# Performance work log

Measured on AMD Instinct MI355X. Metric: run time of the kernel, lower is better.

The kernel has to match this reference:

```python
import jax, jax.numpy as jnp
import numpy as np

H = 516      # LSTM hidden per direction
T = 512      # encoder source length
B = 64       # batch
NY = 20      # decoder target length
SEQ = 20     # seqLen == decoder input feature == n classes


def _u(key, shape, k):
    return jax.random.uniform(key, shape, jnp.float32, -k, k)


def setup_inputs() -> dict:
    key = jax.random.key(0)
    ks = jax.random.split(key, 26)
    kh = float(1.0 / np.sqrt(H))
    ka = float(1.0 / np.sqrt(2 * H * 2))
    inp = {}
    inp['x'] = jax.random.normal(ks[0], (T, B, 4), jnp.float32)
    inp['y'] = jax.random.normal(ks[1], (NY, B, SEQ), jnp.float32)
    inp['label'] = jax.random.randint(ks[2], (NY, B), 0, SEQ)
    inp['expand_W'] = _u(ks[3], (256, 4), 0.5)
    inp['expand_b'] = _u(ks[4], (256,), 0.5)
    # encoder biLSTM: 2 layers x 2 directions; PyTorch gate order i,f,g,o
    inp['eWi0'] = _u(ks[5], (2, 4 * H, 256), kh)
    inp['eWh0'] = _u(ks[6], (2, 4 * H, H), kh)
    inp['eb0'] = _u(ks[7], (2, 4 * H), kh)
    inp['eWi1'] = _u(ks[8], (2, 4 * H, 2 * H), kh)
    inp['eWh1'] = _u(ks[9], (2, 4 * H, H), kh)
    inp['eb1'] = _u(ks[10], (2, 4 * H), kh)
    # decoder biLSTM
    inp['dWi0'] = _u(ks[11], (2, 4 * H, SEQ), kh)
    inp['dWh0'] = _u(ks[12], (2, 4 * H, H), kh)
    inp['db0'] = _u(ks[13], (2, 4 * H), kh)
    inp['dWi1'] = _u(ks[14], (2, 4 * H, 2 * H), kh)
    inp['dWh1'] = _u(ks[15], (2, 4 * H, H), kh)
    inp['db1'] = _u(ks[16], (2, 4 * H), kh)
    # concat attention: Linear(2064, 1032) + v
    inp['attn_W'] = _u(ks[17], (2 * H, 4 * H), ka)
    inp['attn_b'] = _u(ks[18], (2 * H,), ka)
    inp['attn_v'] = _u(ks[19], (2 * H,), ka)
    inp['concat_W'] = _u(ks[20], (2 * H, 4 * H), ka)
    inp['concat_b'] = _u(ks[21], (2 * H,), ka)
    inp['out_W'] = _u(ks[22], (SEQ, 2 * H), float(1.0 / np.sqrt(2 * H)))
    inp['out_b'] = _u(ks[23], (SEQ,), float(1.0 / np.sqrt(2 * H)))
    return inp


def _cell(x, h, c, Wi, Wh, b):
    g = x @ Wi.T + h @ Wh.T + b
    i, f, gg, o = jnp.split(g, 4, axis=-1)
    c2 = jax.nn.sigmoid(f) * c + jax.nn.sigmoid(i) * jnp.tanh(gg)
    h2 = jax.nn.sigmoid(o) * jnp.tanh(c2)
    return h2, c2


def _run_dir(xs, h0, c0, Wi, Wh, b, reverse):
    def step(carry, xt):
        h, c = _cell(xt, carry[0], carry[1], Wi, Wh, b)
        return (h, c), h
    (hT, cT), ys = jax.lax.scan(step, (h0, c0), xs, reverse=reverse)
    return ys, hT, cT


def _bilstm(xs, Wi0, Wh0, b0, Wi1, Wh1, b1):
    z = jnp.zeros((xs.shape[1], H), xs.dtype)
    out = xs
    hs, cs = [], []
    for Wi, Wh, b in ((Wi0, Wh0, b0), (Wi1, Wh1, b1)):
        yf, hf, cf = _run_dir(out, z, z, Wi[0], Wh[0], b[0], False)
        yb, hb, cb = _run_dir(out, z, z, Wi[1], Wh[1], b[1], True)
        out = jnp.concatenate([yf, yb], -1)
        hs += [hf, hb]
        cs += [cf, cb]
    return out, jnp.stack(hs), jnp.stack(cs)


def reference(x, y, label, expand_W, expand_b, eWi0, eWh0, eb0, eWi1, eWh1, eb1,
              dWi0, dWh0, db0, dWi1, dWh1, db1, attn_W, attn_b, attn_v,
              concat_W, concat_b, out_W, out_b):
    xe = x @ expand_W.T + expand_b                       # [T,B,256]
    outenc, h0, c0 = _bilstm(xe, eWi0, eWh0, eb0, eWi1, eWh1, eb1)  # [T,B,1032],[4,B,H]
    lab = label.astype(jnp.int32)

    def dec_step(carry, inp):
        h, c, loss = carry
        yi, li = inp                                    # [B,SEQ], [B]
        # 1-step bidirectional 2-layer decoder LSTM (seq len 1 => fwd==bwd path)
        h0f, c0f = _cell(yi, h[0], c[0], dWi0[0], dWh0[0], db0[0])
        h0b, c0b = _cell(yi, h[1], c[1], dWi0[1], dWh0[1], db0[1])
        l0 = jnp.concatenate([h0f, h0b], -1)
        h1f, c1f = _cell(l0, h[2], c[2], dWi1[0], dWh1[0], db1[0])
        h1b, c1b = _cell(l0, h[3], c[3], dWi1[1], dWh1[1], db1[1])
        outdec = jnp.concatenate([h1f, h1b], -1)        # [B,1032]
        # concat attention over encoder outputs
        hid = jnp.broadcast_to(outdec[None], outenc.shape)
        energy = jnp.tanh(jnp.concatenate([hid, outenc], -1) @ attn_W.T + attn_b)
        score = jnp.einsum('h,tbh->tb', attn_v, energy)
        aw = jax.nn.softmax(score, axis=0)              # softmax over src_len
        context = jnp.einsum('tb,tbh->bh', aw, outenc)
        co = jnp.tanh(jnp.concatenate([outdec, context], -1) @ concat_W.T + concat_b)
        logits = co @ out_W.T + out_b                   # [B,SEQ]
        ls = jax.nn.log_softmax(logits, -1)
        ce = -jnp.take_along_axis(ls, li[:, None], 1).mean()
        h_new = jnp.stack([h0f, h0b, h1f, h1b])
        c_new = jnp.stack([c0f, c0b, c1f, c1b])
        return (h_new, c_new, loss + ce), None

    init = (h0, c0, jnp.float32(0.0))
    (_, _, loss), _ = jax.lax.scan(dec_step, init, (y, lab))
    return loss
```

## Files before the change

### kernel.cpp

```cpp
#include <hip/hip_runtime.h>
#include <hip/hip_bf16.h>
#include <cstdint>

typedef __attribute__((ext_vector_type(8))) short s8v;
typedef __attribute__((ext_vector_type(4))) float f4v;

#define DEV __device__ __forceinline__

constexpr int Hh  = 516;
constexpr int HP  = 544;
constexpr int FH  = 2064;
constexpr int NP  = 2176;
constexpr int TT  = 512;
constexpr int BB  = 64;
constexpr int LD2 = 1088;
constexpr int LDE = 1152;
constexpr int CS  = 528;
constexpr int XR  = 584;

DEV float bf2f(unsigned short u){ return __builtin_bit_cast(float, (unsigned)u<<16); }
DEV unsigned short f2bf(float f){
  unsigned u = __builtin_bit_cast(unsigned, f);
  u += 0x7fffu + ((u>>16)&1u);
  return (unsigned short)(u>>16);
}
DEV float sigf(float x){ return 1.f/(1.f+__expf(-x)); }
DEV float tanhfast(float x){ float e=__expf(2.f*x); return 1.f - 2.f/(e+1.f); }

DEV void cell_x1(f4v (&acc)[4],
                 const unsigned short* __restrict__ X1, int ld1,
                 const unsigned short* __restrict__ W1, int ldw1, int K1,
                 int j0)
{
  const int tid = threadIdx.x;
  const int w = tid>>6, lane = tid&63, p = lane&15, q = lane>>4;
  const unsigned short* wrow = W1 + (size_t)(w*HP + j0 + p)*ldw1 + q*8;
  for (int kk = 0; kk < (K1>>5); ++kk) {
    s8v bfr = *(const s8v*)(wrow + (size_t)kk*32);
    #pragma unroll
    for (int m = 0; m < 4; ++m) {
      s8v afr = *(const s8v*)(X1 + (size_t)(m*16+p)*ld1 + kk*32 + q*8);
      acc[m] = __builtin_amdgcn_mfma_f32_16x16x32_bf16(afr, bfr, acc[m], 0, 0, 0);
    }
  }
}

template<bool AST>
DEV void cell_rest(f4v (&acc)[4],
                   const unsigned short* __restrict__ X2g, int ldx2,
                   const unsigned short* __restrict__ W2,
                   const float* __restrict__ bias,
                   float* __restrict__ cst,
                   unsigned short* __restrict__ hout,
                   unsigned short* __restrict__ yout, int ldy, int ycol,
                   int j0)
{
  __shared__ __align__(16) unsigned short Xs[64*XR];
  __shared__ float gbuf[4][64][17];
  const int tid = threadIdx.x;
  const int w = tid>>6, lane = tid&63, p = lane&15, q = lane>>4;

  {
    int r = tid >> 2, c = tid & 3;
    const char* src = (const char*)X2g + (size_t)r*(ldx2*2) + c*16;
    char* dst = (char*)Xs + (size_t)r*(XR*2) + c*16;
    s8v tmp[17];
    #pragma unroll
    for (int k = 0; k < 17; ++k) tmp[k] = *(const s8v*)(src + (size_t)k*64);
    #pragma unroll
    for (int k = 0; k < 17; ++k) *(s8v*)(dst + k*64) = tmp[k];
  }
  __syncthreads();

  {
    const unsigned short* wrow = W2 + (size_t)(w*HP + j0 + p)*HP + q*8;
    #pragma unroll
    for (int kk = 0; kk < HP/32; ++kk) {
      s8v bfr = *(const s8v*)(wrow + kk*32);
      #pragma unroll
      for (int m = 0; m < 4; ++m) {
        s8v afr = *(const s8v*)(Xs + (m*16+p)*XR + kk*32 + q*8);
        acc[m] = __builtin_amdgcn_mfma_f32_16x16x32_bf16(afr, bfr, acc[m], 0, 0, 0);
      }
    }
  }
  {
    int j = j0 + p;
    float bval = (j < Hh) ? bias[w*Hh + j] : 0.f;
    #pragma unroll
    for (int m = 0; m < 4; ++m)
      #pragma unroll
      for (int r = 0; r < 4; ++r)
        gbuf[w][m*16 + q*4 + r][p] = acc[m][r] + bval;
  }
  __syncthreads();
  {
    int b = tid & 63, j4 = tid >> 6;
    unsigned short hb[4];
    #pragma unroll
    for (int ii = 0; ii < 4; ++ii) {
      int jj = j4*4 + ii, jg = j0 + jj;
      float gi = gbuf[0][b][jj], gf = gbuf[1][b][jj];
      float gg = gbuf[2][b][jj], go = gbuf[3][b][jj];
      bool valid = jg < Hh;
      float c  = valid ? cst[(size_t)b*CS + jg] : 0.f;
      float c2 = sigf(gf)*c + sigf(gi)*tanhfast(gg);
      float h  = sigf(go)*tanhfast(c2);
      if (valid) cst[(size_t)b*CS + jg] = c2;
      hb[ii] = valid ? f2bf(h) : (unsigned short)0;
    }
    unsigned hu0 = (unsigned)hb[0] | ((unsigned)hb[1] << 16);
    unsigned hu1 = (unsigned)hb[2] | ((unsigned)hb[3] << 16);
    unsigned long long yv = (unsigned long long)hu0 | ((unsigned long long)hu1 << 32);
    unsigned long long* yp =
      (unsigned long long*)(yout + (size_t)b*ldy + ycol + j0 + j4*4);
    if (AST)
      __hip_atomic_store(yp, yv, __ATOMIC_RELAXED, __HIP_MEMORY_SCOPE_AGENT);
    else
      *yp = yv;
    if (hout)
      *(unsigned long long*)(hout + (size_t)b*HP + j0 + j4*4) = yv;
  }
  __syncthreads();
}

__global__ void __launch_bounds__(256) enc_rnn(
  const unsigned short* __restrict__ Wi,
  int ldwi, int K1,
  const unsigned short* __restrict__ Xseq,
  int ld1,
  const unsigned short* __restrict__ Wh,
  const float* __restrict__ eb,
  unsigned short* __restrict__ yout,
  const unsigned short* __restrict__ hz,
  float* __restrict__ cst,
  unsigned* __restrict__ flags)
{
  int d = blockIdx.x / 33, slot = blockIdx.x % 33, j0 = slot * 16;
  const unsigned short* W1 = Wi + (size_t)d*NP*ldwi;
  const unsigned short* W2 = Wh + (size_t)d*NP*HP;
  const float* bias = eb + (size_t)d*FH;
  float* cs = cst + (size_t)d*BB*CS;
  unsigned* flg = flags + (size_t)d*TT*64;
  for (int t = 0; t < TT; ++t) {
    int tf = d ? (TT-1-t) : t;
    f4v acc[4] = {};
    cell_x1(acc, Xseq + (size_t)tf*BB*ld1, ld1, W1, ldwi, K1, j0);
    if (t > 0 && threadIdx.x < 64) {
      const unsigned* f = flg + (size_t)(t-1)*64;
      while (true) {
        unsigned v = (threadIdx.x < 33)
          ? __hip_atomic_load(f + threadIdx.x, __ATOMIC_RELAXED, __HIP_MEMORY_SCOPE_AGENT)
          : 1u;
        if (__all((int)(v != 0))) break;
        __builtin_amdgcn_s_sleep(1);
      }
    }
    __syncthreads();
    const unsigned short* X2g; int ldx2;
    if (t == 0) { X2g = hz; ldx2 = HP; }
    else {
      int tp = d ? (TT - t) : (t - 1);
      X2g = yout + (size_t)tp*BB*LD2 + d*HP; ldx2 = LD2;
    }
    cell_rest<true>(acc, X2g, ldx2, W2, bias, cs, nullptr,
                    yout + (size_t)tf*BB*LD2, LD2, d*HP, j0);
    if (threadIdx.x == 0)
      __hip_atomic_store(flg + (size_t)t*64 + slot, 1u,
                         __ATOMIC_RELAXED, __HIP_MEMORY_SCOPE_AGENT);
  }
}

__global__ void __launch_bounds__(256) dec_cell(
  const unsigned short* __restrict__ X1, int ld1, int K1,
  const unsigned short* __restrict__ hin_base,
  unsigned short* __restrict__ hout_base,
  int loff,
  const unsigned short* __restrict__ Wi, int ldwi,
  const unsigned short* __restrict__ Whh,
  const float* __restrict__ dbias,
  float* __restrict__ cstates,
  unsigned short* __restrict__ yout, int ldy)
{
  int d = blockIdx.x / 33, j0 = (blockIdx.x % 33) * 16;
  f4v acc[4] = {};
  cell_x1(acc, X1, ld1, Wi + (size_t)d*NP*ldwi, ldwi, K1, j0);
  cell_rest<false>(acc,
    hin_base + (size_t)(loff+d)*BB*HP, HP,
    Whh + (size_t)d*NP*HP,
    dbias + (size_t)d*FH,
    cstates + (size_t)(loff+d)*BB*CS,
    hout_base + (size_t)(loff+d)*BB*HP,
    yout, ldy, d*HP, j0);
}

__global__ void __launch_bounds__(256) gemm_bt(
  const unsigned short* __restrict__ A, int lda,
  const unsigned short* __restrict__ W, int ldw,
  unsigned short* __restrict__ C, int ldc, int K,
  const float* __restrict__ bias, int nbias)
{
  __shared__ __align__(16) unsigned short As[128*72];
  __shared__ __align__(16) unsigned short Ws[128*72];
  int tid = threadIdx.x, w = tid>>6, lane = tid&63, p = lane&15, q = lane>>4;
  int wm = w & 1, wn = w >> 1;
  size_t m0 = (size_t)blockIdx.x * 128;
  int n0 = blockIdx.y * 128;
  f4v acc[4][4] = {};
  for (int k0 = 0; k0 < K; k0 += 64) {
    __syncthreads();
    #pragma unroll
    for (int i = 0; i < 4; ++i) {
      int v = tid + i*256;
      int row = v >> 3, k8 = (v & 7) * 8;
      *(s8v*)(As + row*72 + k8) = *(const s8v*)(A + (m0+row)*lda + k0 + k8);
      *(s8v*)(Ws + row*72 + k8) = *(const s8v*)(W + (size_t)(n0+row)*ldw + k0 + k8);
    }
    __syncthreads();
    #pragma unroll
    for (int kk = 0; kk < 2; ++kk) {
      s8v af[4], bf[4];
      #pragma unroll
      for (int i = 0; i < 4; ++i) {
        af[i] = *(const s8v*)(As + (wm*64 + i*16 + p)*72 + kk*32 + q*8);
        bf[i] = *(const s8v*)(Ws + (wn*64 + i*16 + p)*72 + kk*32 + q*8);
      }
      #pragma unroll
      for (int mt = 0; mt < 4; ++mt)
        #pragma unroll
        for (int nt = 0; nt < 4; ++nt)
          acc[mt][nt] = __builtin_amdgcn_mfma_f32_16x16x32_bf16(af[mt], bf[nt], acc[mt][nt], 0,0,0);
    }
  }
  #pragma unroll
  for (int mt = 0; mt < 4; ++mt)
    #pragma unroll
    for (int nt = 0; nt < 4; ++nt)
      #pragma unroll
      for (int r = 0; r < 4; ++r) {
        size_t row = m0 + wm*64 + mt*16 + q*4 + r;
        int col = n0 + wn*64 + nt*16 + p;
        float v = acc[mt][nt][r];
        if (bias && col < nbias) v += bias[col];
        C[row*ldc + col] = f2bf(v);
      }
}

__global__ void __launch_bounds__(256) gemm64(
  const unsigned short* __restrict__ A, int lda,
  const unsigned short* __restrict__ W, int ldw, int K,
  const float* __restrict__ bias, int nbias, int mode,
  void* __restrict__ C, int ldc)
{
  int tid = threadIdx.x, w = tid>>6, lane = tid&63, p = lane&15, q = lane>>4;
  int n0 = blockIdx.x*64 + w*16;
  f4v acc[4] = {};
  const unsigned short* wrow = W + (size_t)(n0+p)*ldw + q*8;
  for (int kk = 0; kk < K/32; ++kk) {
    s8v bfr = *(const s8v*)(wrow + kk*32);
    #pragma unroll
    for (int m = 0; m < 4; ++m) {
      s8v afr = *(const s8v*)(A + (size_t)(m*16+p)*lda + kk*32 + q*8);
      acc[m] = __builtin_amdgcn_mfma_f32_16x16x32_bf16(afr, bfr, acc[m], 0,0,0);
    }
  }
  #pragma unroll
  for (int m = 0; m < 4; ++m)
    #pragma unroll
    for (int r = 0; r < 4; ++r) {
      int b = m*16 + q*4 + r, col = n0 + p;
      float v = acc[m][r];
      if (bias && col < nbias) v += bias[col];
      if (mode == 2) v = tanhfast(v);
      if (mode == 0) ((float*)C)[(size_t)b*ldc + col] = v;
      else ((unsigned short*)C)[(size_t)b*ldc + col] = f2bf(v);
    }
}

__global__ void __launch_bounds__(256) attn_score(
  const unsigned short* __restrict__ encp,
  const float* __restrict__ qv,
  const float* __restrict__ av,
  float* __restrict__ score)
{
  int t = blockIdx.x;
  int w = threadIdx.x>>6, lane = threadIdx.x&63;
  float vv[17];
  #pragma unroll
  for (int i = 0; i < 17; ++i) { int n = i*64+lane; vv[i] = (n < 1032) ? av[n] : 0.f; }
  const unsigned short* erow = encp + (size_t)t*BB*LDE;
  for (int bb = 0; bb < 16; ++bb) {
    int b = w*16 + bb;
    const unsigned short* e = erow + (size_t)b*LDE;
    const float* qb = qv + (size_t)b*LDE;
    float s = 0.f;
    #pragma unroll
    for (int i = 0; i < 17; ++i) {
      int n = i*64 + lane;
      s += vv[i] * tanhfast(bf2f(e[n]) + qb[n]);
    }
    #pragma unroll
    for (int off = 32; off; off >>= 1) s += __shfl_xor(s, off);
    if (lane == 0) score[(size_t)t*BB + b] = s;
  }
}

__global__ void __launch_bounds__(256) attn_ctx(
  const float* __restrict__ score,
  const unsigned short* __restrict__ outenc,
  unsigned short* __restrict__ Xc)
{
  __shared__ float aw[512];
  __shared__ float red[4];
  int tid = threadIdx.x, w = tid>>6, lane = tid&63;
  int b = blockIdx.x >> 1, half = blockIdx.x & 1;
  float s0 = score[(size_t)tid*BB + b];
  float s1 = score[(size_t)(tid+256)*BB + b];
  float m = fmaxf(s0, s1);
  #pragma unroll
  for (int off = 32; off; off >>= 1) m = fmaxf(m, __shfl_xor(m, off));
  if (lane == 0) red[w] = m;
  __syncthreads();
  m = fmaxf(fmaxf(red[0], red[1]), fmaxf(red[2], red[3]));
  __syncthreads();
  float e0 = __expf(s0 - m), e1 = __expf(s1 - m);
  aw[tid] = e0; aw[tid+256] = e1;
  float ss = e0 + e1;
  #pragma unroll
  for (int off = 32; off; off >>= 1) ss += __shfl_xor(ss, off);
  if (lane == 0) red[w] = ss;
  __syncthreads();
  float inv = 1.f / (red[0]+red[1]+red[2]+red[3]);
  float acc0 = 0.f, acc1 = 0.f, acc2 = 0.f;
  const unsigned short* base = outenc + (size_t)b*LD2 + half*HP;
  for (int t = 0; t < 512; ++t) {
    float a_ = aw[t];
    const unsigned short* orow = base + (size_t)t*BB*LD2;
    acc0 += a_ * bf2f(orow[tid]);
    acc1 += a_ * bf2f(orow[tid+256]);
    if (tid < 32) acc2 += a_ * bf2f(orow[tid+512]);
  }
  unsigned short* dst = Xc + (size_t)b*2176 + 1088 + half*HP;
  dst[tid]      = f2bf(acc0*inv);
  dst[tid+256]  = f2bf(acc1*inv);
  if (tid < 32) dst[tid+512] = f2bf(acc2*inv);
}

__global__ void ce_k(const float* __restrict__ logits,
                     const int* __restrict__ label,
                     float* __restrict__ out)
{
  int b = threadIdx.x;
  const float* lr = logits + (size_t)b*64;
  float m = -1e30f;
  for (int n = 0; n < 20; ++n) m = fmaxf(m, lr[n]);
  float s = 0.f;
  for (int n = 0; n < 20; ++n) s += __expf(lr[n] - m);
  int li = label[b];
  float ce = -(lr[li] - m - __logf(s));
  #pragma unroll
  for (int off = 32; off; off >>= 1) ce += __shfl_xor(ce, off);
  if (b == 0) atomicAdd(out, ce * (1.f/64.f));
}

__global__ void __launch_bounds__(256) expand_k(
  const float* __restrict__ x, const float* __restrict__ eW,
  const float* __restrict__ ebi, unsigned short* __restrict__ xe)
{
  int row = blockIdx.x, j = threadIdx.x;
  const float* xr = x + (size_t)row*4;
  float4 wv = ((const float4*)eW)[j];
  float v = ebi[j] + xr[0]*wv.x + xr[1]*wv.y + xr[2]*wv.z + xr[3]*wv.w;
  xe[(size_t)row*256 + j] = f2bf(v);
}

__global__ void __launch_bounds__(256) dec_init(
  const unsigned short* __restrict__ y0,
  const unsigned short* __restrict__ oenc,
  const float* __restrict__ encC,
  unsigned short* __restrict__ decH,
  float* __restrict__ decC)
{
  int tid = blockIdx.x*256 + threadIdx.x;
  int nth = gridDim.x*256;
  for (int i = tid; i < 4*BB*HP; i += nth) {
    int k = i / (BB*HP), rem = i % (BB*HP);
    int b = rem / HP, j = rem % HP;
    const unsigned short* src = (k < 2) ? y0 : oenc;
    int t = (k & 1) ? 0 : (TT-1);
    decH[i] = src[(size_t)t*BB*LD2 + (size_t)b*LD2 + (k&1)*HP + j];
  }
  for (int i = tid; i < 4*BB*CS; i += nth) {
    int k = i / (BB*CS), rem = i % (BB*CS);
    decC[i] = encC[((size_t)(k>>1)*2 + (k&1))*BB*CS + rem];
  }
}

struct PackA {
  const float *eWi0,*eWh0,*eWi1,*eWh1,*dWi0,*dWh0,*dWi1,*dWh1,*aW,*cW,*oW,*y;
  unsigned short *pEWi0,*pEWh0,*pEWi1,*pEWh1,*pDWi0,*pDWh0,*pDWi1,*pDWh1,
                 *pAW1,*pAW2,*pCW,*pOW,*pY;
};

__global__ void __launch_bounds__(256) pack_k(PackA a){
  int job = blockIdx.y, row = blockIdx.x, tid = threadIdx.x;
  if (job < 16) {
    if (row >= NP) return;
    int d = job & 1, jt = job >> 1;
    int g = row / HP, jj = row % HP; bool vr = jj < Hh; int sr = g*Hh + jj;
    if (jt == 0) {
      unsigned short* dst = a.pEWi0 + ((size_t)d*NP + row)*256;
      const float* s = a.eWi0 + ((size_t)d*FH + sr)*256;
      for (int k = tid; k < 256; k += 256) dst[k] = vr ? f2bf(s[k]) : 0;
    } else if (jt == 1) {
      unsigned short* dst = a.pEWh0 + ((size_t)d*NP + row)*HP;
      const float* s = a.eWh0 + ((size_t)d*FH + sr)*Hh;
      for (int k = tid; k < HP; k += 256) dst[k] = (vr && k < Hh) ? f2bf(s[k]) : 0;
    } else if (jt == 2) {
      unsigned short* dst = a.pEWi1 + ((size_t)d*NP + row)*LD2;
      const float* s = a.eWi1 + ((size_t)d*FH + sr)*1032;
      for (int k = tid; k < LD2; k += 256) {
        int d2 = k/HP, j = k%HP;
        dst[k] = (vr && j < Hh) ? f2bf(s[d2*Hh + j]) : 0;
      }
    } else if (jt == 3) {
      unsigned short* dst = a.pEWh1 + ((size_t)d*NP + row)*HP;
      const float* s = a.eWh1 + ((size_t)d*FH + sr)*Hh;
      for (int k = tid; k < HP; k += 256) dst[k] = (vr && k < Hh) ? f2bf(s[k]) : 0;
    } else if (jt == 4) {
      unsigned short* dst = a.pDWi0 + ((size_t)d*NP + row)*64;
      const float* s = a.dWi0 + ((size_t)d*FH + sr)*20;
      for (int k = tid; k < 64; k += 256) dst[k] = (vr && k < 20) ? f2bf(s[k]) : 0;
    } else if (jt == 5) {
      unsigned short* dst = a.pDWh0 + ((size_t)d*NP + row)*HP;
      const float* s = a.dWh0 + ((size_t)d*FH + sr)*Hh;
      for (int k = tid; k < HP; k += 256) dst[k] = (vr && k < Hh) ? f2bf(s[k]) : 0;
    } else if (jt == 6) {
      unsigned short* dst = a.pDWi1 + ((size_t)d*NP + row)*LD2;
      const float* s = a.dWi1 + ((size_t)d*FH + sr)*1032;
      for (int k = tid; k < LD2; k += 256) {
        int d2 = k/HP, j = k%HP;
        dst[k] = (vr && j < Hh) ? f2bf(s[d2*Hh + j]) : 0;
      }
    } else {
      unsigned short* dst = a.pDWh1 + ((size_t)d*NP + row)*HP;
      const float* s = a.dWh1 + ((size_t)d*FH + sr)*Hh;
      for (int k = tid; k < HP; k += 256) dst[k] = (vr && k < Hh) ? f2bf(s[k]) : 0;
    }
  } else if (job == 16 || job == 17) {
    if (row >= LDE) return;
    bool vr = row < 1032;
    unsigned short* dst = (job == 16 ? a.pAW1 : a.pAW2) + (size_t)row*LD2;
    int off = (job == 16 ? 0 : 1032);
    for (int k = tid; k < LD2; k += 256) {
      int d2 = k/HP, j = k%HP;
      dst[k] = (vr && j < Hh) ? f2bf(a.aW[(size_t)row*FH + off + d2*Hh + j]) : 0;
    }
  } else if (job == 18) {
    if (row >= LDE) return;
    bool vr = row < 1032;
    unsigned short* dst = a.pCW + (size_t)row*2176;
    for (int k = tid; k < 2176; k += 256) {
      int half = k/LD2, r2 = k%LD2, d2 = r2/HP, j = r2%HP;
      dst[k] = (vr && j < Hh) ? f2bf(a.cW[(size_t)row*FH + half*1032 + d2*Hh + j]) : 0;
    }
  } else if (job == 19) {
    if (row >= 64) return;
    unsigned short* dst = a.pOW + (size_t)row*LD2;
    for (int k = tid; k < LD2; k += 256)
      dst[k] = (row < 20 && k < 1032) ? f2bf(a.oW[(size_t)row*1032 + k]) : 0;
  } else {
    if (row >= 1280) return;
    unsigned short* dst = a.pY + (size_t)row*64;
    for (int k = tid; k < 64; k += 256)
      dst[k] = (k < 20) ? f2bf(a.y[(size_t)row*20 + k]) : 0;
  }
}

extern "C" void kernel_launch(void* const* d_in, const int* in_sizes, int n_in,
                              void* d_out, int out_size, void* d_ws, size_t ws_size,
                              hipStream_t stream) {
  const float* x    = (const float*)d_in[0];
  const float* y    = (const float*)d_in[1];
  const int* label  = (const int*)d_in[2];
  const float* expW = (const float*)d_in[3];
  const float* expb = (const float*)d_in[4];
  const float* eWi0 = (const float*)d_in[5];
  const float* eWh0 = (const float*)d_in[6];
  const float* eb0  = (const float*)d_in[7];
  const float* eWi1 = (const float*)d_in[8];
  const float* eWh1 = (const float*)d_in[9];
  const float* eb1  = (const float*)d_in[10];
  const float* dWi0 = (const float*)d_in[11];
  const float* dWh0 = (const float*)d_in[12];
  const float* db0  = (const float*)d_in[13];
  const float* dWi1 = (const float*)d_in[14];
  const float* dWh1 = (const float*)d_in[15];
  const float* db1  = (const float*)d_in[16];
  const float* attW = (const float*)d_in[17];
  const float* attb = (const float*)d_in[18];
  const float* attv = (const float*)d_in[19];
  const float* cW   = (const float*)d_in[20];
  const float* cb   = (const float*)d_in[21];
  const float* oW   = (const float*)d_in[22];
  const float* ob   = (const float*)d_in[23];

  char* base = (char*)d_ws;
  size_t o = 0;
  auto alloc = [&](size_t bytes){ size_t r = o; o = (o + bytes + 255) & ~(size_t)255; return r; };

  size_t o_hz    = alloc((size_t)BB*HP*2);
  size_t o_decH  = alloc((size_t)2*4*BB*HP*2);
  size_t o_l0    = alloc((size_t)BB*LD2*2);
  size_t o_Xc    = alloc((size_t)BB*2176*2);
  size_t o_encC  = alloc((size_t)2*2*BB*CS*4);
  size_t o_decC  = alloc((size_t)4*BB*CS*4);
  size_t o_flags = alloc((size_t)2*2*TT*64*4);
  size_t ZB = o;
  size_t o_xe    = alloc((size_t)TT*BB*256*2);
  size_t o_big   = alloc((size_t)TT*BB*LDE*2);
  size_t o_oenc  = alloc((size_t)TT*BB*LD2*2);
  size_t o_pEWi0 = alloc((size_t)2*NP*256*2);
  size_t o_pEWh0 = alloc((size_t)2*NP*HP*2);
  size_t o_pEWi1 = alloc((size_t)2*NP*LD2*2);
  size_t o_pEWh1 = alloc((size_t)2*NP*HP*2);
  size_t o_pDWi0 = alloc((size_t)2*NP*64*2);
  size_t o_pDWh0 = alloc((size_t)2*NP*HP*2);
  size_t o_pDWi1 = alloc((size_t)2*NP*LD2*2);
  size_t o_pDWh1 = alloc((size_t)2*NP*HP*2);
  size_t o_pAW1  = alloc((size_t)LDE*LD2*2);
  size_t o_pAW2  = alloc((size_t)LDE*LD2*2);
  size_t o_pCW   = alloc((size_t)LDE*2176*2);
  size_t o_pOW   = alloc((size_t)64*LD2*2);
  size_t o_pY    = alloc((size_t)1280*64*2);
  size_t o_q     = alloc((size_t)BB*LDE*4);
  size_t o_score = alloc((size_t)TT*BB*4);
  size_t o_co    = alloc((size_t)BB*LD2*2);
  size_t o_log   = alloc((size_t)BB*64*4);
  (void)in_sizes; (void)n_in; (void)out_size;

  if (o > ws_size) return;

  unsigned short* hz   = (unsigned short*)(base + o_hz);
  unsigned short* decH = (unsigned short*)(base + o_decH);
  unsigned short* l0   = (unsigned short*)(base + o_l0);
  unsigned short* Xc   = (unsigned short*)(base + o_Xc);
  float* encC = (float*)(base + o_encC);
  float* decC = (float*)(base + o_decC);
  unsigned* flags = (unsigned*)(base + o_flags);
  unsigned short* xe   = (unsigned short*)(base + o_xe);
  unsigned short* y0   = (unsigned short*)(base + o_big);
  unsigned short* encp = (unsigned short*)(base + o_big);
  unsigned short* oenc = (unsigned short*)(base + o_oenc);
  unsigned short* pEWi0 = (unsigned short*)(base + o_pEWi0);
  unsigned short* pEWh0 = (unsigned short*)(base + o_pEWh0);
  unsigned short* pEWi1 = (unsigned short*)(base + o_pEWi1);
  unsigned short* pEWh1 = (unsigned short*)(base + o_pEWh1);
  unsigned short* pDWi0 = (unsigned short*)(base + o_pDWi0);
  unsigned short* pDWh0 = (unsigned short*)(base + o_pDWh0);
  unsigned short* pDWi1 = (unsigned short*)(base + o_pDWi1);
  unsigned short* pDWh1 = (unsigned short*)(base + o_pDWh1);
  unsigned short* pAW1 = (unsigned short*)(base + o_pAW1);
  unsigned short* pAW2 = (unsigned short*)(base + o_pAW2);
  unsigned short* pCW  = (unsigned short*)(base + o_pCW);
  unsigned short* pOW  = (unsigned short*)(base + o_pOW);
  unsigned short* pY   = (unsigned short*)(base + o_pY);
  float* qbuf  = (float*)(base + o_q);
  float* score = (float*)(base + o_score);
  unsigned short* co = (unsigned short*)(base + o_co);
  float* logits = (float*)(base + o_log);

  hipMemsetAsync(d_ws, 0, ZB, stream);
  hipMemsetAsync(d_out, 0, sizeof(float), stream);

  PackA pa;
  pa.eWi0 = eWi0; pa.eWh0 = eWh0; pa.eWi1 = eWi1; pa.eWh1 = eWh1;
  pa.dWi0 = dWi0; pa.dWh0 = dWh0; pa.dWi1 = dWi1; pa.dWh1 = dWh1;
  pa.aW = attW; pa.cW = cW; pa.oW = oW; pa.y = y;
  pa.pEWi0 = pEWi0; pa.pEWh0 = pEWh0; pa.pEWi1 = pEWi1; pa.pEWh1 = pEWh1;
  pa.pDWi0 = pDWi0; pa.pDWh0 = pDWh0; pa.pDWi1 = pDWi1; pa.pDWh1 = pDWh1;
  pa.pAW1 = pAW1; pa.pAW2 = pAW2; pa.pCW = pCW; pa.pOW = pOW; pa.pY = pY;
  pack_k<<<dim3(NP, 21), 256, 0, stream>>>(pa);

  expand_k<<<TT*BB, 256, 0, stream>>>(x, expW, expb, xe);

  enc_rnn<<<66, 256, 0, stream>>>(pEWi0, 256, 256, xe, 256,
      pEWh0, eb0, y0, hz, encC, flags);
  enc_rnn<<<66, 256, 0, stream>>>(pEWi1, LD2, LD2, y0, LD2,
      pEWh1, eb1, oenc, hz, encC + (size_t)2*BB*CS, flags + (size_t)2*TT*64);

  dec_init<<<64, 256, 0, stream>>>(y0, oenc, encC, decH, decC);

  gemm_bt<<<dim3(256, 9), 256, 0, stream>>>(
      oenc, LD2, pAW2, LD2, encp, LDE, LD2, attb, 1032);

  const size_t DHB = (size_t)4*BB*HP;
  for (int s = 0; s < 20; ++s) {
    int p = s & 1, p2 = p ^ 1;
    dec_cell<<<66, 256, 0, stream>>>(
      pY + (size_t)s*64*64, 64, 64, decH + (size_t)p*DHB, decH + (size_t)p2*DHB, 0,
      pDWi0, 64, pDWh0, db0, decC, l0, LD2);
    dec_cell<<<66, 256, 0, stream>>>(
      l0, LD2, LD2, decH + (size_t)p*DHB, decH + (size_t)p2*DHB, 2,
      pDWi1, LD2, pDWh1, db1, decC, Xc, 2176);
    gemm64<<<18, 256, 0, stream>>>(Xc, 2176, pAW1, LD2, LD2, nullptr, 0, 0, qbuf, LDE);
    attn_score<<<512, 256, 0, stream>>>(encp, qbuf, attv, score);
    attn_ctx<<<128, 256, 0, stream>>>(score, oenc, Xc);
    gemm64<<<17, 256, 0, stream>>>(Xc, 2176, pCW, 2176, 2176, cb, 1032, 2, co, LD2);
    gemm64<<<1, 256, 0, stream>>>(co, LD2, pOW, LD2, LD2, ob, 20, 0, logits, 64);
    ce_k<<<1, 64, 0, stream>>>(logits, label + (size_t)s*64, (float*)d_out);
  }
}
```

Baseline: 24.34 ms.

## Replace persistent flag-synced encoder kernel with per-timestep launches and widen padded layouts

The persistent encoder RNN kernel, which synchronised blocks across timesteps by spinning on global flags, is replaced by one kernel launch per timestep. Stream ordering now provides the inter-step dependency, which removes the atomic flag polling and the atomic stores. The concatenated bidirectional buffers are repadded from 544 to 576 per direction (row stride 1152, concat width 2304), and the packed weights and consumers are updated to match. The cost is 1024 extra kernel launches, each paying launch latency and reloading weights. The wider padding also adds wasted MFMA work on the zero columns.

```diff
diff --git a/kernel.cpp b/kernel.cpp
--- a/kernel.cpp
+++ b/kernel.cpp
@@ -9,11 +9,13 @@
 
 constexpr int Hh  = 516;
 constexpr int HP  = 544;
+constexpr int HPL = 576;
 constexpr int FH  = 2064;
 constexpr int NP  = 2176;
 constexpr int TT  = 512;
 constexpr int BB  = 64;
-constexpr int LD2 = 1088;
+constexpr int LD2B= 1152;
+constexpr int XCW = 2304;
 constexpr int LDE = 1152;
 constexpr int CS  = 528;
 constexpr int XR  = 584;
@@ -45,7 +47,6 @@
   }
 }
 
-template<bool AST>
 DEV void cell_rest(f4v (&acc)[4],
                    const unsigned short* __restrict__ X2g, int ldx2,
                    const unsigned short* __restrict__ W2,
@@ -112,19 +113,13 @@
     unsigned hu0 = (unsigned)hb[0] | ((unsigned)hb[1] << 16);
     unsigned hu1 = (unsigned)hb[2] | ((unsigned)hb[3] << 16);
     unsigned long long yv = (unsigned long long)hu0 | ((unsigned long long)hu1 << 32);
-    unsigned long long* yp =
-      (unsigned long long*)(yout + (size_t)b*ldy + ycol + j0 + j4*4);
-    if (AST)
-      __hip_atomic_store(yp, yv, __ATOMIC_RELAXED, __HIP_MEMORY_SCOPE_AGENT);
-    else
-      *yp = yv;
+    *(unsigned long long*)(yout + (size_t)b*ldy + ycol + j0 + j4*4) = yv;
     if (hout)
       *(unsigned long long*)(hout + (size_t)b*HP + j0 + j4*4) = yv;
   }
-  __syncthreads();
-}
-
-__global__ void __launch_bounds__(256) enc_rnn(
+}
+
+__global__ void __launch_bounds__(256) enc_step(
   const unsigned short* __restrict__ Wi,
   int ldwi, int K1,
   const unsigned short* __restrict__ Xseq,
@@ -134,41 +129,23 @@
   unsigned short* __restrict__ yout,
   const unsigned short* __restrict__ hz,
   float* __restrict__ cst,
-  unsigned* __restrict__ flags)
-{
-  int d = blockIdx.x / 33, slot = blockIdx.x % 33, j0 = slot * 16;
-  const unsigned short* W1 = Wi + (size_t)d*NP*ldwi;
-  const unsigned short* W2 = Wh + (size_t)d*NP*HP;
-  const float* bias = eb + (size_t)d*FH;
-  float* cs = cst + (size_t)d*BB*CS;
-  unsigned* flg = flags + (size_t)d*TT*64;
-  for (int t = 0; t < TT; ++t) {
-    int tf = d ? (TT-1-t) : t;
-    f4v acc[4] = {};
-    cell_x1(acc, Xseq + (size_t)tf*BB*ld1, ld1, W1, ldwi, K1, j0);
-    if (t > 0 && threadIdx.x < 64) {
-      const unsigned* f = flg + (size_t)(t-1)*64;
-      while (true) {
-        unsigned v = (threadIdx.x < 33)
-          ? __hip_atomic_load(f + threadIdx.x, __ATOMIC_RELAXED, __HIP_MEMORY_SCOPE_AGENT)
-          : 1u;
-        if (__all((int)(v != 0))) break;
-        __builtin_amdgcn_s_sleep(1);
-      }
-    }
-    __syncthreads();
-    const unsigned short* X2g; int ldx2;
-    if (t == 0) { X2g = hz; ldx2 = HP; }
-    else {
-      int tp = d ? (TT - t) : (t - 1);
-      X2g = yout + (size_t)tp*BB*LD2 + d*HP; ldx2 = LD2;
-    }
-    cell_rest<true>(acc, X2g, ldx2, W2, bias, cs, nullptr,
-                    yout + (size_t)tf*BB*LD2, LD2, d*HP, j0);
-    if (threadIdx.x == 0)
-      __hip_atomic_store(flg + (size_t)t*64 + slot, 1u,
-                         __ATOMIC_RELAXED, __HIP_MEMORY_SCOPE_AGENT);
-  }
+  int t)
+{
+  int d = blockIdx.x / 33, j0 = (blockIdx.x % 33) * 16;
+  int tf = d ? (TT-1-t) : t;
+  f4v acc[4] = {};
+  cell_x1(acc, Xseq + (size_t)tf*BB*ld1, ld1,
+          Wi + (size_t)d*NP*ldwi, ldwi, K1, j0);
+  const unsigned short* X2g;
+  if (t == 0) X2g = hz;
+  else {
+    int tp = d ? (TT - t) : (t - 1);
+    X2g = yout + (size_t)tp*BB*LD2B + d*HPL;
+  }
+  cell_rest(acc, X2g, LD2B,
+            Wh + (size_t)d*NP*HP, eb + (size_t)d*FH,
+            cst + (size_t)d*BB*CS, nullptr,
+            yout + (size_t)tf*BB*LD2B, LD2B, d*HPL, j0);
 }
 
 __global__ void __launch_bounds__(256) dec_cell(
@@ -185,13 +162,13 @@
   int d = blockIdx.x / 33, j0 = (blockIdx.x % 33) * 16;
   f4v acc[4] = {};
   cell_x1(acc, X1, ld1, Wi + (size_t)d*NP*ldwi, ldwi, K1, j0);
-  cell_rest<false>(acc,
+  cell_rest(acc,
     hin_base + (size_t)(loff+d)*BB*HP, HP,
     Whh + (size_t)d*NP*HP,
     dbias + (size_t)d*FH,
     cstates + (size_t)(loff+d)*BB*CS,
     hout_base + (size_t)(loff+d)*BB*HP,
-    yout, ldy, d*HP, j0);
+    yout, ldy, d*HPL, j0);
 }
 
 __global__ void __launch_bounds__(256) gemm_bt(
@@ -285,9 +262,9 @@
 {
   int t = blockIdx.x;
   int w = threadIdx.x>>6, lane = threadIdx.x&63;
-  float vv[17];
+  float vv[18];
   #pragma unroll
-  for (int i = 0; i < 17; ++i) { int n = i*64+lane; vv[i] = (n < 1032) ? av[n] : 0.f; }
+  for (int i = 0; i < 18; ++i) { int n = i*64+lane; vv[i] = (n < 1032) ? av[n] : 0.f; }
   const unsigned short* erow = encp + (size_t)t*BB*LDE;
   for (int bb = 0; bb < 16; ++bb) {
     int b = w*16 + bb;
@@ -295,7 +272,7 @@
     const float* qb = qv + (size_t)b*LDE;
     float s = 0.f;
     #pragma unroll
-    for (int i = 0; i < 17; ++i) {
+    for (int i = 0; i < 18; ++i) {
       int n = i*64 + lane;
       s += vv[i] * tanhfast(bf2f(e[n]) + qb[n]);
     }
@@ -332,15 +309,15 @@
   __syncthreads();
   float inv = 1.f / (red[0]+red[1]+red[2]+red[3]);
   float acc0 = 0.f, acc1 = 0.f, acc2 = 0.f;
-  const unsigned short* base = outenc + (size_t)b*LD2 + half*HP;
+  const unsigned short* base = outenc + (size_t)b*LD2B + half*HPL;
   for (int t = 0; t < 512; ++t) {
     float a_ = aw[t];
-    const unsigned short* orow = base + (size_t)t*BB*LD2;
+    const unsigned short* orow = base + (size_t)t*BB*LD2B;
     acc0 += a_ * bf2f(orow[tid]);
     acc1 += a_ * bf2f(orow[tid+256]);
     if (tid < 32) acc2 += a_ * bf2f(orow[tid+512]);
   }
-  unsigned short* dst = Xc + (size_t)b*2176 + 1088 + half*HP;
+  unsigned short* dst = Xc + (size_t)b*XCW + 1152 + half*HPL;
   dst[tid]      = f2bf(acc0*inv);
   dst[tid+256]  = f2bf(acc1*inv);
   if (tid < 32) dst[tid+512] = f2bf(acc2*inv);
@@ -388,7 +365,7 @@
     int b = rem / HP, j = rem % HP;
     const unsigned short* src = (k < 2) ? y0 : oenc;
     int t = (k & 1) ? 0 : (TT-1);
-    decH[i] = src[(size_t)t*BB*LD2 + (size_t)b*LD2 + (k&1)*HP + j];
+    decH[i] = src[(size_t)t*BB*LD2B + (size_t)b*LD2B + (k&1)*HPL + j];
   }
   for (int i = tid; i < 4*BB*CS; i += nth) {
     int k = i / (BB*CS), rem = i % (BB*CS);
@@ -417,10 +394,10 @@
       const float* s = a.eWh0 + ((size_t)d*FH + sr)*Hh;
       for (int k = tid; k < HP; k += 256) dst[k] = (vr && k < Hh) ? f2bf(s[k]) : 0;
     } else if (jt == 2) {
-      unsigned short* dst = a.pEWi1 + ((size_t)d*NP + row)*LD2;
+      unsigned short* dst = a.pEWi1 + ((size_t)d*NP + row)*LD2B;
       const float* s = a.eWi1 + ((size_t)d*FH + sr)*1032;
-      for (int k = tid; k < LD2; k += 256) {
-        int d2 = k/HP, j = k%HP;
+      for (int k = tid; k < LD2B; k += 256) {
+        int d2 = k/HPL, j = k%HPL;
         dst[k] = (vr && j < Hh) ? f2bf(s[d2*Hh + j]) : 0;
       }
     } else if (jt == 3) {
@@ -436,10 +413,10 @@
       const float* s = a.dWh0 + ((size_t)d*FH + sr)*Hh;
       for (int k = tid; k < HP; k += 256) dst[k] = (vr && k < Hh) ? f2bf(s[k]) : 0;
     } else if (jt == 6) {
-      unsigned short* dst = a.pDWi1 + ((size_t)d*NP + row)*LD2;
+      unsigned short* dst = a.pDWi1 + ((size_t)d*NP + row)*LD2B;
       const float* s = a.dWi1 + ((size_t)d*FH + sr)*1032;
-      for (int k = tid; k < LD2; k += 256) {
-        int d2 = k/HP, j = k%HP;
+      for (int k = tid; k < LD2B; k += 256) {
+        int d2 = k/HPL, j = k%HPL;
         dst[k] = (vr && j < Hh) ? f2bf(s[d2*Hh + j]) : 0;
       }
     } else {
@@ -450,24 +427,24 @@
   } else if (job == 16 || job == 17) {
     if (row >= LDE) return;
     bool vr = row < 1032;
-    unsigned short* dst = (job == 16 ? a.pAW1 : a.pAW2) + (size_t)row*LD2;
+    unsigned short* dst = (job == 16 ? a.pAW1 : a.pAW2) + (size_t)row*LD2B;
     int off = (job == 16 ? 0 : 1032);
-    for (int k = tid; k < LD2; k += 256) {
-      int d2 = k/HP, j = k%HP;
+    for (int k = tid; k < LD2B; k += 256) {
+      int d2 = k/HPL, j = k%HPL;
       dst[k] = (vr && j < Hh) ? f2bf(a.aW[(size_t)row*FH + off + d2*Hh + j]) : 0;
     }
   } else if (job == 18) {
     if (row >= LDE) return;
     bool vr = row < 1032;
-    unsigned short* dst = a.pCW + (size_t)row*2176;
-    for (int k = tid; k < 2176; k += 256) {
-      int half = k/LD2, r2 = k%LD2, d2 = r2/HP, j = r2%HP;
+    unsigned short* dst = a.pCW + (size_t)row*XCW;
+    for (int k = tid; k < XCW; k += 256) {
+      int half = k/1152, r2 = k%1152, d2 = r2/HPL, j = r2%HPL;
       dst[k] = (vr && j < Hh) ? f2bf(a.cW[(size_t)row*FH + half*1032 + d2*Hh + j]) : 0;
     }
   } else if (job == 19) {
     if (row >= 64) return;
-    unsigned short* dst = a.pOW + (size_t)row*LD2;
-    for (int k = tid; k < LD2; k += 256)
+    unsigned short* dst = a.pOW + (size_t)row*1088;
+    for (int k = tid; k < 1088; k += 256)
       dst[k] = (row < 20 && k < 1032) ? f2bf(a.oW[(size_t)row*1032 + k]) : 0;
   } else {
     if (row >= 1280) return;
@@ -509,33 +486,32 @@
   size_t o = 0;
   auto alloc = [&](size_t bytes){ size_t r = o; o = (o + bytes + 255) & ~(size_t)255; return r; };
 
-  size_t o_hz    = alloc((size_t)BB*HP*2);
+  size_t o_hz    = alloc((size_t)BB*LD2B*2);
   size_t o_decH  = alloc((size_t)2*4*BB*HP*2);
-  size_t o_l0    = alloc((size_t)BB*LD2*2);
-  size_t o_Xc    = alloc((size_t)BB*2176*2);
+  size_t o_l0    = alloc((size_t)BB*LD2B*2);
+  size_t o_Xc    = alloc((size_t)BB*XCW*2);
   size_t o_encC  = alloc((size_t)2*2*BB*CS*4);
   size_t o_decC  = alloc((size_t)4*BB*CS*4);
-  size_t o_flags = alloc((size_t)2*2*TT*64*4);
   size_t ZB = o;
   size_t o_xe    = alloc((size_t)TT*BB*256*2);
-  size_t o_big   = alloc((size_t)TT*BB*LDE*2);
-  size_t o_oenc  = alloc((size_t)TT*BB*LD2*2);
+  size_t o_big   = alloc((size_t)TT*BB*LD2B*2);
+  size_t o_oenc  = alloc((size_t)TT*BB*LD2B*2);
   size_t o_pEWi0 = alloc((size_t)2*NP*256*2);
   size_t o_pEWh0 = alloc((size_t)2*NP*HP*2);
-  size_t o_pEWi1 = alloc((size_t)2*NP*LD2*2);
+  size_t o_pEWi1 = alloc((size_t)2*NP*LD2B*2);
   size_t o_pEWh1 = alloc((size_t)2*NP*HP*2);
   size_t o_pDWi0 = alloc((size_t)2*NP*64*2);
   size_t o_pDWh0 = alloc((size_t)2*NP*HP*2);
-  size_t o_pDWi1 = alloc((size_t)2*NP*LD2*2);
+  size_t o_pDWi1 = alloc((size_t)2*NP*LD2B*2);
   size_t o_pDWh1 = alloc((size_t)2*NP*HP*2);
-  size_t o_pAW1  = alloc((size_t)LDE*LD2*2);
-  size_t o_pAW2  = alloc((size_t)LDE*LD2*2);
-  size_t o_pCW   = alloc((size_t)LDE*2176*2);
-  size_t o_pOW   = alloc((size_t)64*LD2*2);
+  size_t o_pAW1  = alloc((size_t)LDE*LD2B*2);
+  size_t o_pAW2  = alloc((size_t)LDE*LD2B*2);
+  size_t o_pCW   = alloc((size_t)LDE*XCW*2);
+  size_t o_pOW   = alloc((size_t)64*1088*2);
   size_t o_pY    = alloc((size_t)1280*64*2);
   size_t o_q     = alloc((size_t)BB*LDE*4);
   size_t o_score = alloc((size_t)TT*BB*4);
-  size_t o_co    = alloc((size_t)BB*LD2*2);
+  size_t o_co    = alloc((size_t)BB*1088*2);
   size_t o_log   = alloc((size_t)BB*64*4);
   (void)in_sizes; (void)n_in; (void)out_size;
 
@@ -547,7 +523,6 @@
   unsigned short* Xc   = (unsigned short*)(base + o_Xc);
   float* encC = (float*)(base + o_encC);
   float* decC = (float*)(base + o_decC);
-  unsigned* flags = (unsigned*)(base + o_flags);
   unsigned short* xe   = (unsigned short*)(base + o_xe);
   unsigned short* y0   = (unsigned short*)(base + o_big);
   unsigned short* encp = (unsigned short*)(base + o_big);
@@ -584,30 +559,32 @@
 
   expand_k<<<TT*BB, 256, 0, stream>>>(x, expW, expb, xe);
 
-  enc_rnn<<<66, 256, 0, stream>>>(pEWi0, 256, 256, xe, 256,
-      pEWh0, eb0, y0, hz, encC, flags);
-  enc_rnn<<<66, 256, 0, stream>>>(pEWi1, LD2, LD2, y0, LD2,
-      pEWh1, eb1, oenc, hz, encC + (size_t)2*BB*CS, flags + (size_t)2*TT*64);
+  for (int t = 0; t < TT; ++t)
+    enc_step<<<66, 256, 0, stream>>>(pEWi0, 256, 256, xe, 256,
+        pEWh0, eb0, y0, hz, encC, t);
+  for (int t = 0; t < TT; ++t)
+    enc_step<<<66, 256, 0, stream>>>(pEWi1, LD2B, LD2B, y0, LD2B,
+        pEWh1, eb1, oenc, hz, encC + (size_t)2*BB*CS, t);
 
   dec_init<<<64, 256, 0, stream>>>(y0, oenc, encC, decH, decC);
 
   gemm_bt<<<dim3(256, 9), 256, 0, stream>>>(
-      oenc, LD2, pAW2, LD2, encp, LDE, LD2, attb, 1032);
+      oenc, LD2B, pAW2, LD2B, encp, LDE, LD2B, attb, 1032);
 
   const size_t DHB = (size_t)4*BB*HP;
   for (int s = 0; s < 20; ++s) {
     int p = s & 1, p2 = p ^ 1;
     dec_cell<<<66, 256, 0, stream>>>(
       pY + (size_t)s*64*64, 64, 64, decH + (size_t)p*DHB, decH + (size_t)p2*DHB, 0,
-      pDWi0, 64, pDWh0, db0, decC, l0, LD2);
+      pDWi0, 64, pDWh0, db0, decC, l0, LD2B);
     dec_cell<<<66, 256, 0, stream>>>(
-      l0, LD2, LD2, decH + (size_t)p*DHB, decH + (size_t)p2*DHB, 2,
-      pDWi1, LD2, pDWh1, db1, decC, Xc, 2176);
-    gemm64<<<18, 256, 0, stream>>>(Xc, 2176, pAW1, LD2, LD2, nullptr, 0, 0, qbuf, LDE);
+      l0, LD2B, LD2B, decH + (size_t)p*DHB, decH + (size_t)p2*DHB, 2,
+      pDWi1, LD2B, pDWh1, db1, decC, Xc, XCW);
+    gemm64<<<18, 256, 0, stream>>>(Xc, XCW, pAW1, LD2B, LD2B, nullptr, 0, 0, qbuf, LDE);
     attn_score<<<512, 256, 0, stream>>>(encp, qbuf, attv, score);
     attn_ctx<<<128, 256, 0, stream>>>(score, oenc, Xc);
-    gemm64<<<17, 256, 0, stream>>>(Xc, 2176, pCW, 2176, 2176, cb, 1032, 2, co, LD2);
-    gemm64<<<1, 256, 0, stream>>>(co, LD2, pOW, LD2, LD2, ob, 20, 0, logits, 64);
+    gemm64<<<17, 256, 0, stream>>>(Xc, XCW, pCW, XCW, XCW, cb, 1032, 2, co, 1088);
+    gemm64<<<1, 256, 0, stream>>>(co, 1088, pOW, 1088, 1088, ob, 20, 0, logits, 64);
     ce_k<<<1, 64, 0, stream>>>(logits, label + (size_t)s*64, (float*)d_out);
   }
 }
```

After: 27.35 ms. 12.3% more time.
